# Kernel tuning notes

Measured on AMD Instinct MI355X. Metric: run time of the kernel, lower is better.

Reference implementation:

```python
import jax, jax.numpy as jnp
import numpy as np
import math

B, L, DIM, H = 2, 2048, 512, 8


def setup_inputs() -> dict:
    key = jax.random.key(0)
    ks = jax.random.split(key, 8)
    s = 0.02
    return {
        "x": jax.random.normal(ks[0], (B, L, DIM), dtype=jnp.float32),
        "Wq": jax.random.normal(ks[1], (DIM, DIM), dtype=jnp.float32) * s,
        "Wk": jax.random.normal(ks[2], (DIM, DIM), dtype=jnp.float32) * s,
        "Wv": jax.random.normal(ks[3], (DIM, DIM), dtype=jnp.float32) * s,
        "Wb": jax.random.normal(ks[4], (H, DIM), dtype=jnp.float32) * s,   # content_bias weight
        "mixing": jax.random.normal(ks[5], (H, DIM), dtype=jnp.float32) * 0.2,  # UNIFORM init, std=0.2
        "Wd": jax.random.normal(ks[6], (DIM, DIM), dtype=jnp.float32) * s,
        "bd": jax.random.normal(ks[7], (DIM,), dtype=jnp.float32) * s,
    }


def reference(x, Wq, Wk, Wv, Wb, mixing, Wd, bd):
    b, l, d = x.shape
    h = mixing.shape[0]
    dh = d // h
    q = x @ Wq.T                      # [B,L,D]
    k = x @ Wk.T                      # [B,S,D]
    v = (x @ Wv.T).reshape(b, l, h, dh).transpose(0, 2, 1, 3)  # [B,H,S,dh]
    # scores[b,h,l,s] = sum_d q[b,l,d] * mixing[h,d] * k[b,s,d]
    scores = jnp.einsum("bld,hd,bsd->bhls", q, mixing, k)
    # content bias: [B,S,H] -> broadcast over query positions as [B,H,1,S]
    cb = jnp.einsum("bsd,hd->bhs", x, Wb)
    scale = math.sqrt(d / h)  # attention_head_size = dim / num_heads
    scores = (scores + cb[:, :, None, :]) / scale
    probs = jax.nn.softmax(scores, axis=-1)   # dropout disabled (eval)
    ctx = jnp.einsum("bhls,bhsd->bhld", probs, v)  # [B,H,L,dh]
    ctx = ctx.transpose(0, 2, 1, 3).reshape(b, l, d)
    return ctx @ Wd.T + bd
```

## Files before the change

kernel.cpp:

```cpp
#include <hip/hip_runtime.h>

#define B_ 2
#define L_ 2048
#define D_ 512
#define H_ 8
#define S_ 2048

typedef __attribute__((ext_vector_type(8))) short short8;
typedef __attribute__((ext_vector_type(8))) unsigned short ushort8;
typedef __attribute__((ext_vector_type(4))) unsigned short ushort4v;
typedef __attribute__((ext_vector_type(4))) float f32x4;
typedef __attribute__((ext_vector_type(16))) float f32x16;
typedef __attribute__((ext_vector_type(4))) float float4v;

__device__ __forceinline__ unsigned short f2bf(float f) {
    unsigned u = __float_as_uint(f);
    u += 0x7FFF + ((u >> 16) & 1);
    return (unsigned short)(u >> 16);
}
__device__ __forceinline__ float bf2f(unsigned short s) {
    return __uint_as_float(((unsigned)s) << 16);
}
__device__ __forceinline__ unsigned char f2fp8(float f) {
    return (unsigned char)(__builtin_amdgcn_cvt_pk_fp8_f32(f, f, 0, false) & 0xff);
}
__device__ __forceinline__ long pack8fp8(const float* v) {
    int lo = __builtin_amdgcn_cvt_pk_fp8_f32(v[0], v[1], 0, false);
    lo = __builtin_amdgcn_cvt_pk_fp8_f32(v[2], v[3], lo, true);
    int hi = __builtin_amdgcn_cvt_pk_fp8_f32(v[4], v[5], 0, false);
    hi = __builtin_amdgcn_cvt_pk_fp8_f32(v[6], v[7], hi, true);
    union { int i[2]; long l; } u;
    u.i[0] = lo; u.i[1] = hi;
    return u.l;
}
__device__ __forceinline__ int swap23(int x) {
    return (x & ~12) | ((x & 4) << 1) | ((x & 8) >> 1);
}
__device__ __forceinline__ void async16(void* lds, const void* g) {
    __builtin_amdgcn_global_load_lds(
        (const __attribute__((address_space(1))) void*)(g),
        (__attribute__((address_space(3))) void*)(lds), 16, 0, 0);
}

__global__ __launch_bounds__(256) void cvt_cb(const float* __restrict__ x,
                                              const float* __restrict__ w0, const float* __restrict__ w1,
                                              const float* __restrict__ w2, const float* __restrict__ w3,
                                              const float* __restrict__ Wb,
                                              unsigned short* __restrict__ xb,
                                              unsigned short* __restrict__ d0, unsigned short* __restrict__ d1,
                                              unsigned short* __restrict__ d2, unsigned short* __restrict__ d3,
                                              unsigned short* __restrict__ cb) {
    if (blockIdx.x < 3072) {
        int i = blockIdx.x * 256 + threadIdx.x;
        const float* s;
        unsigned short* d;
        int idx;
        if (i < 524288) { s = x; d = xb; idx = i; }
        else {
            int off = i - 524288;
            int wsel = off >> 16; idx = off & 65535;
            s = (wsel == 0) ? w0 : (wsel == 1) ? w1 : (wsel == 2) ? w2 : w3;
            d = (wsel == 0) ? d0 : (wsel == 1) ? d1 : (wsel == 2) ? d2 : d3;
        }
        float4v v = *(const float4v*)(s + (size_t)idx * 4);
        ushort4v o;
        o[0] = f2bf(v[0]); o[1] = f2bf(v[1]); o[2] = f2bf(v[2]); o[3] = f2bf(v[3]);
        *(ushort4v*)(d + (size_t)idx * 4) = o;
    } else {
        const int tid = threadIdx.x, w = tid >> 6, lane = tid & 63;
        const int row = (blockIdx.x - 3072) * 4 + w;
        const int h = lane >> 3, seg = lane & 7;
        const float* xp = x + (size_t)row * 512 + seg * 64;
        const float* wp = Wb + (size_t)h * 512 + seg * 64;
        float acc = 0.f;
        #pragma unroll
        for (int j = 0; j < 16; ++j) {
            float4v xv = *(const float4v*)(xp + j * 4);
            float4v wv = *(const float4v*)(wp + j * 4);
            acc += xv[0] * wv[0] + xv[1] * wv[1] + xv[2] * wv[2] + xv[3] * wv[3];
        }
        acc += __shfl_xor(acc, 1);
        acc += __shfl_xor(acc, 2);
        acc += __shfl_xor(acc, 4);
        if (seg == 0) {
            int b = row >> 11, s = row & 2047;
            cb[((size_t)(b * H_ + h)) * S_ + s] = f2bf(acc * 0.125f);
        }
    }
}

__device__ __forceinline__ void gemm128_core(const unsigned short* __restrict__ Ap,
                                             const unsigned short* __restrict__ Bp,
                                             short* sA, short* sB, int tid, f32x4 c[4][4]) {
    const int w = tid >> 6, lane = tid & 63, quad = lane >> 4, l15 = lane & 15;
    const int wm = (w >> 1) * 64, wn = (w & 1) * 64;
    for (int kc = 0; kc < 8; ++kc) {
        __syncthreads();
        #pragma unroll
        for (int j = 0; j < 4; ++j) {
            int i = tid + j * 256;
            int row = i >> 3, seg = i & 7;
            *(ushort8*)&sA[row * 72 + seg * 8] = *(const ushort8*)(Ap + (size_t)row * 512 + kc * 64 + seg * 8);
            *(ushort8*)&sB[row * 72 + seg * 8] = *(const ushort8*)(Bp + (size_t)row * 512 + kc * 64 + seg * 8);
        }
        __syncthreads();
        #pragma unroll
        for (int ks = 0; ks < 2; ++ks) {
            short8 a[4], b[4];
            #pragma unroll
            for (int ii = 0; ii < 4; ++ii)
                a[ii] = *(const short8*)&sA[(wm + ii * 16 + l15) * 72 + ks * 32 + quad * 8];
            #pragma unroll
            for (int jj = 0; jj < 4; ++jj)
                b[jj] = *(const short8*)&sB[(wn + jj * 16 + l15) * 72 + ks * 32 + quad * 8];
            #pragma unroll
            for (int ii = 0; ii < 4; ++ii)
                #pragma unroll
                for (int jj = 0; jj < 4; ++jj)
                    c[ii][jj] = __builtin_amdgcn_mfma_f32_16x16x32_bf16(a[ii], b[jj], c[ii][jj], 0, 0, 0);
        }
    }
}

__global__ __launch_bounds__(256) void gemm_qkv(const unsigned short* __restrict__ xb,
                                                const unsigned short* __restrict__ Wqb,
                                                const unsigned short* __restrict__ Wkb,
                                                const unsigned short* __restrict__ Wvb,
                                                unsigned short* __restrict__ qb,
                                                unsigned char* __restrict__ kpack8,
                                                unsigned short* __restrict__ vfrag) {
    __shared__ short sA[128 * 72];
    __shared__ short sB[128 * 72];
    const int m0 = blockIdx.x * 128, n0 = blockIdx.y * 128, z = blockIdx.z;
    const unsigned short* Bsel = (z == 0) ? Wqb : ((z == 1) ? Wkb : Wvb);
    f32x4 c[4][4];
    #pragma unroll
    for (int ii = 0; ii < 4; ++ii)
        #pragma unroll
        for (int jj = 0; jj < 4; ++jj) { f32x4 zv = {0.f, 0.f, 0.f, 0.f}; c[ii][jj] = zv; }
    gemm128_core(xb + (size_t)m0 * 512, Bsel + (size_t)n0 * 512, sA, sB, threadIdx.x, c);
    const int tid = threadIdx.x, w = tid >> 6, lane = tid & 63, quad = lane >> 4, l15 = lane & 15;
    const int wm = (w >> 1) * 64, wn = (w & 1) * 64;
    #pragma unroll
    for (int ii = 0; ii < 4; ++ii) {
        const int mb = m0 + wm + ii * 16 + quad * 4;
        const int bb = mb >> 11;
        if (z == 0) {
            #pragma unroll
            for (int jj = 0; jj < 4; ++jj) {
                int ncol = n0 + wn + jj * 16 + l15;
                #pragma unroll
                for (int r = 0; r < 4; ++r)
                    qb[(size_t)(mb + r) * 512 + ncol] = f2bf(c[ii][jj][r]);
            }
        } else if (z == 1) {
            #pragma unroll
            for (int jj = 0; jj < 4; ++jj) {
                int d = n0 + wn + jj * 16 + l15;
                int pair = d >> 5, fh = (d >> 4) & 1, hid = (d >> 3) & 1, jq = d & 7;
                #pragma unroll
                for (int r = 0; r < 4; ++r) {
                    int s = (mb + r) & 2047;
                    int t = s >> 5, rr = swap23(s & 31);
                    kpack8[(((size_t)(bb * 64 + t) * 16 + pair) << 10)
                           + (hid * 32 + rr) * 16 + fh * 8 + jq] = f2fp8(c[ii][jj][r] * 32.f);
                }
            }
        } else {
            const int hh = (n0 + wn) >> 6;
            const int s = mb & 2047;
            #pragma unroll
            for (int jj = 0; jj < 4; ++jj) {
                int dh = jj * 16 + l15;
                ushort4v o;
                o[0] = f2bf(c[ii][jj][0]); o[1] = f2bf(c[ii][jj][1]);
                o[2] = f2bf(c[ii][jj][2]); o[3] = f2bf(c[ii][jj][3]);
                size_t blk = ((size_t)(bb * H_ + hh) * 64 + (s >> 5)) * 4
                           + ((dh >> 5) * 2 + ((s >> 4) & 1));
                *(ushort4v*)(vfrag + blk * 512 + (dh & 31) * 8 + ((s >> 3) & 1) * 256 + (s & 7)) = o;
            }
        }
    }
}

__global__ __launch_bounds__(256) void gemm_out(const unsigned short* __restrict__ ctxb,
                                                const unsigned short* __restrict__ Wdb,
                                                const float* __restrict__ bd,
                                                float* __restrict__ out) {
    __shared__ short sA[128 * 72];
    __shared__ short sB[128 * 72];
    const int m0 = blockIdx.x * 128, n0 = blockIdx.y * 128;
    f32x4 c[4][4];
    #pragma unroll
    for (int ii = 0; ii < 4; ++ii)
        #pragma unroll
        for (int jj = 0; jj < 4; ++jj) { f32x4 zv = {0.f, 0.f, 0.f, 0.f}; c[ii][jj] = zv; }
    gemm128_core(ctxb + (size_t)m0 * 512, Wdb + (size_t)n0 * 512, sA, sB, threadIdx.x, c);
    const int tid = threadIdx.x, w = tid >> 6, lane = tid & 63, quad = lane >> 4, l15 = lane & 15;
    const int wm = (w >> 1) * 64, wn = (w & 1) * 64;
    #pragma unroll
    for (int ii = 0; ii < 4; ++ii) {
        const int mb = m0 + wm + ii * 16 + quad * 4;
        #pragma unroll
        for (int jj = 0; jj < 4; ++jj) {
            int ncol = n0 + wn + jj * 16 + l15;
            float bias = bd[ncol];
            #pragma unroll
            for (int r = 0; r < 4; ++r)
                out[(size_t)(mb + r) * 512 + ncol] = c[ii][jj][r] + bias;
        }
    }
}

__global__ __launch_bounds__(256, 2) void flash_attn(const unsigned short* __restrict__ qb,
                                                     const unsigned char* __restrict__ kpack8,
                                                     const unsigned short* __restrict__ vfrag,
                                                     const unsigned short* __restrict__ cb_all,
                                                     const float* __restrict__ mixing,
                                                     _Float16* __restrict__ Opart,
                                                     float* __restrict__ lpart) {
    __shared__ char sK[4][8192];
    const int bid = blockIdx.x;
    const int half = bid & 1, b = (bid >> 1) & 1, h = (bid >> 2) & 7, qt = bid >> 5;
    const int tid = threadIdx.x, w = tid >> 6, lane = tid & 63;
    const int l31 = lane & 31, hi = lane >> 5;
    const int q0 = qt * 128 + w * 32;
    const unsigned short* vfb = vfrag + ((size_t)(b * H_ + h) * 64 + half * 32) * 2048;
    const unsigned short* cbq = cb_all + (size_t)(b * H_ + h) * S_ + half * 1024;
    const float* mixh = mixing + h * D_;

    long qq[32];
    {
        const unsigned short* qrow = qb + ((size_t)(b * L_) + q0 + l31) * D_ + hi * 8;
        #pragma unroll
        for (int i = 0; i < 32; ++i) {
            ushort8 qv = *(const ushort8*)(qrow + i * 16);
            float4v ma = *(const float4v*)(mixh + i * 16 + hi * 8);
            float4v mb = *(const float4v*)(mixh + i * 16 + hi * 8 + 4);
            float v[8];
            v[0] = bf2f(qv[0]) * ma[0] * 16.f;
            v[1] = bf2f(qv[1]) * ma[1] * 16.f;
            v[2] = bf2f(qv[2]) * ma[2] * 16.f;
            v[3] = bf2f(qv[3]) * ma[3] * 16.f;
            v[4] = bf2f(qv[4]) * mb[0] * 16.f;
            v[5] = bf2f(qv[5]) * mb[1] * 16.f;
            v[6] = bf2f(qv[6]) * mb[2] * 16.f;
            v[7] = bf2f(qv[7]) * mb[3] * 16.f;
            qq[i] = pack8fp8(v);
        }
    }
    asm volatile("s_waitcnt vmcnt(0)" ::: "memory");

    f32x16 acco0, acco1;
    #pragma unroll
    for (int i = 0; i < 16; ++i) { acco0[i] = 0.f; acco1[i] = 0.f; }
    float lsum = 0.f;
    f32x16 aA0, aB0, aA1, aB1;
    short8 av00, av01, av10, av11;
    ushort8 cbr0, cbr1, cbr2, cbr3;

    auto stageK = [&](int p) {
        const char* src = (const char*)kpack8 + (((size_t)(b * 64 + half * 32)) << 14) + (size_t)p * 8192;
        char* dst = &sK[p & 3][0];
        #pragma unroll
        for (int ii = 0; ii < 2; ++ii)
            async16(dst + w * 1024 + ii * 4096, src + w * 1024 + ii * 4096 + (size_t)lane * 16);
    };
    auto ldV = [&](int t) {
        const unsigned short* vp = vfb + (size_t)t * 2048 + lane * 8;
        av00 = *(const short8*)(vp);
        av01 = *(const short8*)(vp + 512);
        av10 = *(const short8*)(vp + 1024);
        av11 = *(const short8*)(vp + 1536);
        asm volatile("" ::: "memory");
    };
    auto ldCB = [&](int t) {
        const unsigned short* cp = cbq + t * 32;
        cbr0 = *(const ushort8*)(cp);
        cbr1 = *(const ushort8*)(cp + 8);
        cbr2 = *(const ushort8*)(cp + 16);
        cbr3 = *(const ushort8*)(cp + 24);
        asm volatile("" ::: "memory");
    };
    auto qk_chunk = [&](const char* buf, int qbase, f32x16& A, f32x16& B) {
        __builtin_amdgcn_s_setprio(1);
        #pragma unroll
        for (int p = 0; p < 8; ++p) {
            long a0, a1;
            {
                const long* ap = (const long*)&buf[p * 1024 + lane * 16];
                a0 = ap[0];
                a1 = ap[1];
            }
            A = __builtin_amdgcn_mfma_f32_32x32x16_fp8_fp8(a0, qq[qbase + 2 * p], A, 0, 0, 0);
            B = __builtin_amdgcn_mfma_f32_32x32x16_fp8_fp8(a1, qq[qbase + 2 * p + 1], B, 0, 0, 0);
        }
        __builtin_amdgcn_s_setprio(0);
    };
    auto softmax_pv = [&](const f32x16& A, const f32x16& B) {
        float p[16];
        #pragma unroll
        for (int R = 0; R < 16; ++R) {
            const int cr = (R & 3) + 8 * (R >> 2);
            const int il = cr - 4 * ((R >> 2) & 1);
            const int ih = il + 8;
            unsigned short ca = (il < 8)  ? cbr0[il & 7] : cbr2[il & 7];
            unsigned short cbb = (ih < 16) ? cbr1[ih & 7] : cbr3[ih & 7];
            float cbv = bf2f(hi ? cbb : ca);
            float pe = __expf((A[R] + B[R]) * (1.0f / 4096.0f) + cbv);
            p[R] = pe;
            lsum += pe;
        }
        union { unsigned int u[4]; short8 s8; } P0, P1;
        #pragma unroll
        for (int j = 0; j < 4; ++j) {
            P0.u[j] = __builtin_amdgcn_perm(__float_as_uint(p[2 * j + 1]) + 0x8000u,
                                            __float_as_uint(p[2 * j]) + 0x8000u, 0x07060302u);
            P1.u[j] = __builtin_amdgcn_perm(__float_as_uint(p[8 + 2 * j + 1]) + 0x8000u,
                                            __float_as_uint(p[8 + 2 * j]) + 0x8000u, 0x07060302u);
        }
        __builtin_amdgcn_s_setprio(1);
        acco0 = __builtin_amdgcn_mfma_f32_32x32x16_bf16(av00, P0.s8, acco0, 0, 0, 0);
        acco0 = __builtin_amdgcn_mfma_f32_32x32x16_bf16(av01, P1.s8, acco0, 0, 0, 0);
        acco1 = __builtin_amdgcn_mfma_f32_32x32x16_bf16(av10, P0.s8, acco1, 0, 0, 0);
        acco1 = __builtin_amdgcn_mfma_f32_32x32x16_bf16(av11, P1.s8, acco1, 0, 0, 0);
        __builtin_amdgcn_s_setprio(0);
    };
    auto zero16 = [](f32x16& v) {
        #pragma unroll
        for (int i = 0; i < 16; ++i) v[i] = 0.f;
    };

    stageK(0); stageK(1); stageK(2);

    zero16(aA0); zero16(aB0);
    asm volatile("s_waitcnt vmcnt(4)" ::: "memory");
    __builtin_amdgcn_s_barrier();
    stageK(3);
    qk_chunk(&sK[0][0], 0, aA0, aB0);
    ldV(0); ldCB(0);
    asm volatile("s_waitcnt vmcnt(12)" ::: "memory");
    __builtin_amdgcn_s_barrier();
    stageK(4);
    qk_chunk(&sK[1][0], 16, aA0, aB0);

    #define E_TILE(T, CA, CB, PA, PB)                                            \
        zero16(CA); zero16(CB);                                                  \
        asm volatile("s_waitcnt vmcnt(12)" ::: "memory");       \
        __builtin_amdgcn_s_barrier();                                            \
        stageK(2 * (T) + 3);                                                     \
        qk_chunk(&sK[((T) & 1) << 1][0], 0, CA, CB);                             \
        asm volatile("s_waitcnt vmcnt(4)" ::: "memory");    \
        softmax_pv(PA, PB);                                                      \
        ldV(T); ldCB(T);
    #define O_TILE(T, CA, CB)                                                    \
        __builtin_amdgcn_s_barrier();                                            \
        if ((T) < 30) stageK(2 * (T) + 4);                                       \
        qk_chunk(&sK[(((T) & 1) << 1) | 1][0], 16, CA, CB);

    for (int tt = 1; tt < 30; tt += 2) {
        E_TILE(tt, aA1, aB1, aA0, aB0);
        O_TILE(tt, aA1, aB1);
        E_TILE(tt + 1, aA0, aB0, aA1, aB1);
        O_TILE(tt + 1, aA0, aB0);
    }
    #undef E_TILE
    #undef O_TILE

    {
        zero16(aA1); zero16(aB1);
        asm volatile("s_waitcnt vmcnt(10)" ::: "memory");
        __builtin_amdgcn_s_barrier();
        qk_chunk(&sK[2][0], 0, aA1, aB1);
        asm volatile("s_waitcnt vmcnt(2)" ::: "memory");
        softmax_pv(aA0, aB0);
        ldV(31); ldCB(31);
        asm volatile("s_waitcnt vmcnt(8)" ::: "memory");
        __builtin_amdgcn_s_barrier();
        qk_chunk(&sK[3][0], 16, aA1, aB1);
        asm volatile("s_waitcnt vmcnt(0)" ::: "memory");
        softmax_pv(aA1, aB1);
    }

    lsum += __shfl_xor(lsum, 32);
    if (hi == 0) lpart[(size_t)bid * 128 + w * 32 + l31] = lsum;
    #pragma unroll
    for (int R = 0; R < 16; ++R) {
        int dh = (R & 3) + 8 * (R >> 2) + 4 * hi;
        Opart[((size_t)bid * 64 + dh) * 128 + w * 32 + l31] = (_Float16)acco0[R];
        Opart[((size_t)bid * 64 + 32 + dh) * 128 + w * 32 + l31] = (_Float16)acco1[R];
    }
}

__global__ __launch_bounds__(256) void merge_ctx(const _Float16* __restrict__ Opart,
                                                 const float* __restrict__ lpart,
                                                 unsigned short* __restrict__ ctxb) {
    int t = blockIdx.x * 256 + threadIdx.x;
    int qq = t & 127, dh4 = (t >> 7) & 15, qt = (t >> 11) & 15, h = (t >> 15) & 7, b = t >> 18;
    int base = (qt << 5) | (h << 2) | (b << 1);
    float l = lpart[(size_t)base * 128 + qq] + lpart[(size_t)(base + 1) * 128 + qq];
    float inv = 1.f / l;
    ushort4v o;
    #pragma unroll
    for (int e = 0; e < 4; ++e) {
        int dh = dh4 * 4 + e;
        float v = (float)Opart[((size_t)base * 64 + dh) * 128 + qq]
                + (float)Opart[((size_t)(base + 1) * 64 + dh) * 128 + qq];
        o[e] = f2bf(v * inv);
    }
    *(ushort4v*)(ctxb + ((size_t)(b * L_) + qt * 128 + qq) * 512 + h * 64 + dh4 * 4) = o;
}

extern "C" void kernel_launch(void* const* d_in, const int* in_sizes, int n_in,
                              void* d_out, int out_size, void* d_ws, size_t ws_size,
                              hipStream_t stream) {
    (void)in_sizes; (void)n_in; (void)out_size; (void)ws_size;
    const float* x      = (const float*)d_in[0];
    const float* Wq     = (const float*)d_in[1];
    const float* Wk     = (const float*)d_in[2];
    const float* Wv     = (const float*)d_in[3];
    const float* Wb     = (const float*)d_in[4];
    const float* mixing = (const float*)d_in[5];
    const float* Wd     = (const float*)d_in[6];
    const float* bd     = (const float*)d_in[7];
    float* out = (float*)d_out;

    char* ws = (char*)d_ws;
    const size_t MiB = 1048576;
    unsigned short* xb     = (unsigned short*)(ws);
    unsigned short* qb     = (unsigned short*)(ws + 4 * MiB);
    unsigned char*  kpack8 = (unsigned char*)(ws + 8 * MiB);
    unsigned short* vfrag  = (unsigned short*)(ws + 10 * MiB);
    unsigned short* ctxb   = (unsigned short*)(ws + 14 * MiB);
    unsigned short* Wqb    = (unsigned short*)(ws + 18 * MiB);
    unsigned short* Wkb    = (unsigned short*)(ws + 18 * MiB + 512 * 1024);
    unsigned short* Wvb    = (unsigned short*)(ws + 19 * MiB);
    unsigned short* Wdb    = (unsigned short*)(ws + 19 * MiB + 512 * 1024);
    unsigned short* cbuf   = (unsigned short*)(ws + 20 * MiB);
    float* lpart           = (float*)(ws + 20 * MiB + 256 * 1024);
    _Float16* Opart        = (_Float16*)(ws + 21 * MiB);

    cvt_cb<<<4096, 256, 0, stream>>>(x, Wq, Wk, Wv, Wd, Wb, xb, Wqb, Wkb, Wvb, Wdb, cbuf);
    gemm_qkv<<<dim3(32, 4, 3), 256, 0, stream>>>(xb, Wqb, Wkb, Wvb, qb, kpack8, vfrag);
    flash_attn<<<512, 256, 0, stream>>>(qb, kpack8, vfrag, cbuf, mixing, Opart, lpart);
    merge_ctx<<<2048, 256, 0, stream>>>(Opart, lpart, ctxb);
    gemm_out<<<dim3(32, 4), 256, 0, stream>>>(ctxb, Wdb, bd, out);
}
```

Measured before the change: 200.0 us.

## Interleave softmax exp with QK MFMAs and pre-permute content bias in fp32

The content-bias kernel now writes fp32 values pre-scaled by log2(e) and already permuted into the MFMA accumulator register order. This removes the bf16 unpacking and lane-dependent selects in the attention loop and allows raw v_exp_f32 (exp2) with a single fma. The softmax of the previous tile is fused into the QK chunk loop so the exp and pack VALU work can overlap with the fp8 MFMAs. The wait counts are retuned for the new schedule, which adds some register pressure and doubles the bias buffer size.

```diff
diff --git a/kernel.cpp b/kernel.cpp
--- a/kernel.cpp
+++ b/kernel.cpp
@@ -49,7 +49,7 @@
                                               unsigned short* __restrict__ xb,
                                               unsigned short* __restrict__ d0, unsigned short* __restrict__ d1,
                                               unsigned short* __restrict__ d2, unsigned short* __restrict__ d3,
-                                              unsigned short* __restrict__ cb) {
+                                              float* __restrict__ cbf) {
     if (blockIdx.x < 3072) {
         int i = blockIdx.x * 256 + threadIdx.x;
         const float* s;
@@ -84,7 +84,11 @@
         acc += __shfl_xor(acc, 4);
         if (seg == 0) {
             int b = row >> 11, s = row & 2047;
-            cb[((size_t)(b * H_ + h)) * S_ + s] = f2bf(acc * 0.125f);
+            int T = s >> 5, off = s & 31;
+            int r2 = off & 3, k = off >> 2;
+            int u = (k & 1) + ((k >> 2) << 1), hi2 = (k >> 1) & 1;
+            int R = 4 * u + r2;
+            cbf[((size_t)((b * 8 + h) * 64 + T)) * 32 + hi2 * 16 + R] = acc * 0.125f * 1.44269504f;
         }
     }
 }
@@ -215,7 +219,7 @@
 __global__ __launch_bounds__(256, 2) void flash_attn(const unsigned short* __restrict__ qb,
                                                      const unsigned char* __restrict__ kpack8,
                                                      const unsigned short* __restrict__ vfrag,
-                                                     const unsigned short* __restrict__ cb_all,
+                                                     const float* __restrict__ cbf_all,
                                                      const float* __restrict__ mixing,
                                                      _Float16* __restrict__ Opart,
                                                      float* __restrict__ lpart) {
@@ -226,8 +230,9 @@
     const int l31 = lane & 31, hi = lane >> 5;
     const int q0 = qt * 128 + w * 32;
     const unsigned short* vfb = vfrag + ((size_t)(b * H_ + h) * 64 + half * 32) * 2048;
-    const unsigned short* cbq = cb_all + (size_t)(b * H_ + h) * S_ + half * 1024;
+    const float* cbfb = cbf_all + ((size_t)((b * 8 + h) * 64 + half * 32)) * 32 + hi * 16;
     const float* mixh = mixing + h * D_;
+    const float SC = 1.44269504f / 4096.0f;
 
     long qq[32];
     {
@@ -257,7 +262,7 @@
     float lsum = 0.f;
     f32x16 aA0, aB0, aA1, aB1;
     short8 av00, av01, av10, av11;
-    ushort8 cbr0, cbr1, cbr2, cbr3;
+    float4v cbf0, cbf1, cbf2, cbf3;
 
     auto stageK = [&](int p) {
         const char* src = (const char*)kpack8 + (((size_t)(b * 64 + half * 32)) << 14) + (size_t)p * 8192;
@@ -275,56 +280,78 @@
         asm volatile("" ::: "memory");
     };
     auto ldCB = [&](int t) {
-        const unsigned short* cp = cbq + t * 32;
-        cbr0 = *(const ushort8*)(cp);
-        cbr1 = *(const ushort8*)(cp + 8);
-        cbr2 = *(const ushort8*)(cp + 16);
-        cbr3 = *(const ushort8*)(cp + 24);
+        const float* cp = cbfb + t * 32;
+        cbf0 = *(const float4v*)(cp);
+        cbf1 = *(const float4v*)(cp + 4);
+        cbf2 = *(const float4v*)(cp + 8);
+        cbf3 = *(const float4v*)(cp + 12);
         asm volatile("" ::: "memory");
+    };
+    auto cbfv = [&](int R) -> float {
+        return (R < 4) ? cbf0[R & 3] : (R < 8) ? cbf1[R & 3] : (R < 12) ? cbf2[R & 3] : cbf3[R & 3];
     };
     auto qk_chunk = [&](const char* buf, int qbase, f32x16& A, f32x16& B) {
         __builtin_amdgcn_s_setprio(1);
         #pragma unroll
         for (int p = 0; p < 8; ++p) {
-            long a0, a1;
-            {
-                const long* ap = (const long*)&buf[p * 1024 + lane * 16];
-                a0 = ap[0];
-                a1 = ap[1];
-            }
+            const long* ap = (const long*)&buf[p * 1024 + lane * 16];
+            long a0 = ap[0], a1 = ap[1];
             A = __builtin_amdgcn_mfma_f32_32x32x16_fp8_fp8(a0, qq[qbase + 2 * p], A, 0, 0, 0);
             B = __builtin_amdgcn_mfma_f32_32x32x16_fp8_fp8(a1, qq[qbase + 2 * p + 1], B, 0, 0, 0);
         }
         __builtin_amdgcn_s_setprio(0);
     };
-    auto softmax_pv = [&](const f32x16& A, const f32x16& B) {
-        float p[16];
-        #pragma unroll
-        for (int R = 0; R < 16; ++R) {
-            const int cr = (R & 3) + 8 * (R >> 2);
-            const int il = cr - 4 * ((R >> 2) & 1);
-            const int ih = il + 8;
-            unsigned short ca = (il < 8)  ? cbr0[il & 7] : cbr2[il & 7];
-            unsigned short cbb = (ih < 16) ? cbr1[ih & 7] : cbr3[ih & 7];
-            float cbv = bf2f(hi ? cbb : ca);
-            float pe = __expf((A[R] + B[R]) * (1.0f / 4096.0f) + cbv);
-            p[R] = pe;
-            lsum += pe;
-        }
+    auto pack_pv = [&](const float* pex) {
         union { unsigned int u[4]; short8 s8; } P0, P1;
         #pragma unroll
         for (int j = 0; j < 4; ++j) {
-            P0.u[j] = __builtin_amdgcn_perm(__float_as_uint(p[2 * j + 1]) + 0x8000u,
-                                            __float_as_uint(p[2 * j]) + 0x8000u, 0x07060302u);
-            P1.u[j] = __builtin_amdgcn_perm(__float_as_uint(p[8 + 2 * j + 1]) + 0x8000u,
-                                            __float_as_uint(p[8 + 2 * j]) + 0x8000u, 0x07060302u);
-        }
-        __builtin_amdgcn_s_setprio(1);
+            P0.u[j] = __builtin_amdgcn_perm(__float_as_uint(pex[2 * j + 1]) + 0x8000u,
+                                            __float_as_uint(pex[2 * j]) + 0x8000u, 0x07060302u);
+            P1.u[j] = __builtin_amdgcn_perm(__float_as_uint(pex[8 + 2 * j + 1]) + 0x8000u,
+                                            __float_as_uint(pex[8 + 2 * j]) + 0x8000u, 0x07060302u);
+        }
         acco0 = __builtin_amdgcn_mfma_f32_32x32x16_bf16(av00, P0.s8, acco0, 0, 0, 0);
         acco0 = __builtin_amdgcn_mfma_f32_32x32x16_bf16(av01, P1.s8, acco0, 0, 0, 0);
         acco1 = __builtin_amdgcn_mfma_f32_32x32x16_bf16(av10, P0.s8, acco1, 0, 0, 0);
         acco1 = __builtin_amdgcn_mfma_f32_32x32x16_bf16(av11, P1.s8, acco1, 0, 0, 0);
+    };
+    auto qk_sm = [&](const char* buf, f32x16& CA, f32x16& CB, const f32x16& PA, const f32x16& PB) {
+        __builtin_amdgcn_s_setprio(1);
+        float pex[16];
+        float lsA = 0.f, lsB = 0.f;
+        #pragma unroll
+        for (int p = 0; p < 8; ++p) {
+            const long* ap = (const long*)&buf[p * 1024 + lane * 16];
+            long a0 = ap[0], a1 = ap[1];
+            CA = __builtin_amdgcn_mfma_f32_32x32x16_fp8_fp8(a0, qq[2 * p], CA, 0, 0, 0);
+            CB = __builtin_amdgcn_mfma_f32_32x32x16_fp8_fp8(a1, qq[2 * p + 1], CB, 0, 0, 0);
+            float x0 = fmaf(PA[2 * p] + PB[2 * p], SC, cbfv(2 * p));
+            float x1 = fmaf(PA[2 * p + 1] + PB[2 * p + 1], SC, cbfv(2 * p + 1));
+            float e0, e1;
+            asm("v_exp_f32 %0, %1" : "=v"(e0) : "v"(x0));
+            asm("v_exp_f32 %0, %1" : "=v"(e1) : "v"(x1));
+            pex[2 * p] = e0; pex[2 * p + 1] = e1;
+            lsA += e0; lsB += e1;
+        }
+        lsum += lsA + lsB;
+        pack_pv(pex);
         __builtin_amdgcn_s_setprio(0);
+    };
+    auto sm_pv = [&](const f32x16& PA, const f32x16& PB) {
+        float pex[16];
+        float lsA = 0.f, lsB = 0.f;
+        #pragma unroll
+        for (int R = 0; R < 16; R += 2) {
+            float x0 = fmaf(PA[R] + PB[R], SC, cbfv(R));
+            float x1 = fmaf(PA[R + 1] + PB[R + 1], SC, cbfv(R + 1));
+            float e0, e1;
+            asm("v_exp_f32 %0, %1" : "=v"(e0) : "v"(x0));
+            asm("v_exp_f32 %0, %1" : "=v"(e1) : "v"(x1));
+            pex[R] = e0; pex[R + 1] = e1;
+            lsA += e0; lsB += e1;
+        }
+        lsum += lsA + lsB;
+        pack_pv(pex);
     };
     auto zero16 = [](f32x16& v) {
         #pragma unroll
@@ -344,42 +371,37 @@
     stageK(4);
     qk_chunk(&sK[1][0], 16, aA0, aB0);
 
-    #define E_TILE(T, CA, CB, PA, PB)                                            \
-        zero16(CA); zero16(CB);                                                  \
-        asm volatile("s_waitcnt vmcnt(12)" ::: "memory");       \
-        __builtin_amdgcn_s_barrier();                                            \
-        stageK(2 * (T) + 3);                                                     \
-        qk_chunk(&sK[((T) & 1) << 1][0], 0, CA, CB);                             \
-        asm volatile("s_waitcnt vmcnt(4)" ::: "memory");    \
-        softmax_pv(PA, PB);                                                      \
+    #define E_TILE(T, CA, CB, PA, PB, BK)                                          \
+        zero16(CA); zero16(CB);                                                    \
+        asm volatile("s_waitcnt vmcnt(2)" ::: "memory");                           \
+        __builtin_amdgcn_s_barrier();                                              \
+        stageK(2 * (T) + 3);                                                       \
+        qk_sm(&sK[BK][0], CA, CB, PA, PB);                                         \
         ldV(T); ldCB(T);
-    #define O_TILE(T, CA, CB)                                                    \
-        __builtin_amdgcn_s_barrier();                                            \
-        if ((T) < 30) stageK(2 * (T) + 4);                                       \
-        qk_chunk(&sK[(((T) & 1) << 1) | 1][0], 16, CA, CB);
+    #define O_TILE(T, CA, CB, BK)                                                  \
+        __builtin_amdgcn_s_barrier();                                              \
+        if ((T) < 30) stageK(2 * (T) + 4);                                         \
+        qk_chunk(&sK[BK][0], 16, CA, CB);
 
     for (int tt = 1; tt < 30; tt += 2) {
-        E_TILE(tt, aA1, aB1, aA0, aB0);
-        O_TILE(tt, aA1, aB1);
-        E_TILE(tt + 1, aA0, aB0, aA1, aB1);
-        O_TILE(tt + 1, aA0, aB0);
+        E_TILE(tt, aA1, aB1, aA0, aB0, 2);
+        O_TILE(tt, aA1, aB1, 3);
+        E_TILE(tt + 1, aA0, aB0, aA1, aB1, 0);
+        O_TILE(tt + 1, aA0, aB0, 1);
     }
     #undef E_TILE
     #undef O_TILE
 
     {
         zero16(aA1); zero16(aB1);
-        asm volatile("s_waitcnt vmcnt(10)" ::: "memory");
+        asm volatile("s_waitcnt vmcnt(0)" ::: "memory");
         __builtin_amdgcn_s_barrier();
-        qk_chunk(&sK[2][0], 0, aA1, aB1);
-        asm volatile("s_waitcnt vmcnt(2)" ::: "memory");
-        softmax_pv(aA0, aB0);
+        qk_sm(&sK[2][0], aA1, aB1, aA0, aB0);
         ldV(31); ldCB(31);
-        asm volatile("s_waitcnt vmcnt(8)" ::: "memory");
         __builtin_amdgcn_s_barrier();
         qk_chunk(&sK[3][0], 16, aA1, aB1);
         asm volatile("s_waitcnt vmcnt(0)" ::: "memory");
-        softmax_pv(aA1, aB1);
+        sm_pv(aA1, aB1);
     }
 
     lsum += __shfl_xor(lsum, 32);
@@ -436,7 +458,7 @@
     unsigned short* Wkb    = (unsigned short*)(ws + 18 * MiB + 512 * 1024);
     unsigned short* Wvb    = (unsigned short*)(ws + 19 * MiB);
     unsigned short* Wdb    = (unsigned short*)(ws + 19 * MiB + 512 * 1024);
-    unsigned short* cbuf   = (unsigned short*)(ws + 20 * MiB);
+    float* cbuf            = (float*)(ws + 20 * MiB);
     float* lpart           = (float*)(ws + 20 * MiB + 256 * 1024);
     _Float16* Opart        = (_Float16*)(ws + 21 * MiB);
 
```

After: 201.9 us. Within noise of the previous version (+0.9%).
